# Optimization experiments

Measured on AMD Instinct MI355X. Metric: run time of the kernel, lower is better.

## Reference

```python
import jax, jax.numpy as jnp
import numpy as np
import math

D_MODEL = 512
N_HEADS = 8
WINDOW = 5
B, S = 4, 2048


def setup_inputs() -> dict:
    key = jax.random.key(0)
    ks = jax.random.split(key, 16)
    d = D_MODEL

    def lin(k, fan_in, fan_out):
        bound = 1.0 / math.sqrt(fan_in)
        kw, kb = jax.random.split(k)
        W = jax.random.uniform(kw, (fan_in, fan_out), jnp.float32, -bound, bound)
        b = jax.random.uniform(kb, (fan_out,), jnp.float32, -bound, bound)
        return W, b

    x = jax.random.normal(ks[0], (B, S, d), jnp.float32)
    W1, b1 = lin(ks[1], d, 2 * d)      # mapping layer 1
    W2, b2 = lin(ks[2], 2 * d, d)      # mapping layer 2
    Wq, bq = lin(ks[3], d, d)
    Wk, bk = lin(ks[4], d, d)
    Wv, bv = lin(ks[5], d, d)
    Wo, bo = lin(ks[6], d, d)
    return dict(x=x, W1=W1, b1=b1, W2=W2, b2=b2, Wq=Wq, bq=bq,
                Wk=Wk, bk=bk, Wv=Wv, bv=bv, Wo=Wo, bo=bo)


def reference(x, W1, b1, W2, b2, Wq, bq, Wk, bk, Wv, bv, Wo, bo):
    Bsz, S_, d = x.shape
    h = N_HEADS
    hd = d // h

    # mapping MLP: Linear -> ReLU -> Linear
    xm = jax.nn.relu(x @ W1 + b1) @ W2 + b2

    def split_heads(t):  # [B,S,d] -> [B,h,S,hd]
        return t.reshape(Bsz, S_, h, hd).transpose(0, 2, 1, 3)

    Q = split_heads(xm @ Wq + bq)
    K = split_heads(xm @ Wk + bk)
    V = split_heads(xm @ Wv + bv)

    scores = jnp.einsum('bhqd,bhkd->bhqk', Q, K) / math.sqrt(hd)

    # inverse sliding-window mask: positions with |i-j| <= window are EXCLUDED
    idx = jnp.arange(S_)
    adjacent = jnp.abs(idx[:, None] - idx[None, :]) <= WINDOW  # [S,S] bool
    scores = jnp.where(adjacent[None, None], -1e9, scores)

    attn = jax.nn.softmax(scores, axis=-1)
    out = jnp.einsum('bhqk,bhkd->bhqd', attn, V)
    out = out.transpose(0, 2, 1, 3).reshape(Bsz, S_, d)
    return out @ Wo + bo
```

## Files before the change

kernel.cpp:

```cpp
#include <hip/hip_runtime.h>
#include <stdint.h>

typedef __attribute__((ext_vector_type(8))) short bf16x8;
typedef __attribute__((ext_vector_type(4))) float f32x4;

__device__ __forceinline__ float bf2f(uint16_t u) {
    union { uint32_t u; float f; } c; c.u = ((uint32_t)u) << 16; return c.f;
}
__device__ __forceinline__ uint16_t f2bf(float f) {
    union { float f; uint32_t u; } c; c.f = f;
    uint32_t r = c.u + 0x7fffu + ((c.u >> 16) & 1u);
    return (uint16_t)(r >> 16);
}
__device__ __forceinline__ uint32_t pk2bf(float a, float b) {
#if __has_builtin(__builtin_amdgcn_cvt_pk_bf16_f32)
    auto v = __builtin_amdgcn_cvt_pk_bf16_f32(a, b);
    uint32_t u; __builtin_memcpy(&u, &v, 4); return u;
#else
    return (uint32_t)f2bf(a) | ((uint32_t)f2bf(b) << 16);
#endif
}
__device__ __forceinline__ float fexp2(float x) {
#if __has_builtin(__builtin_amdgcn_exp2f)
    return __builtin_amdgcn_exp2f(x);
#else
    return exp2f(x);
#endif
}

__device__ __forceinline__ void gld_lds16(const uint16_t* g, uint16_t* l) {
    __builtin_amdgcn_global_load_lds(
        (const __attribute__((address_space(1))) void*)g,
        (__attribute__((address_space(3))) void*)l, 16, 0, 0);
}

__global__ void prep_all(const float* __restrict__ x,
                         const float* __restrict__ W1, const float* __restrict__ W2,
                         const float* __restrict__ Wq, const float* __restrict__ Wk,
                         const float* __restrict__ Wv, const float* __restrict__ Wo,
                         const float* __restrict__ b1, const float* __restrict__ b2,
                         const float* __restrict__ bq, const float* __restrict__ bk,
                         const float* __restrict__ bv, const float* __restrict__ bo,
                         uint16_t* __restrict__ W1T, uint16_t* __restrict__ W2T,
                         uint16_t* __restrict__ WqkvT, uint16_t* __restrict__ WoT,
                         uint16_t* __restrict__ xb, uint16_t* __restrict__ bbase)
{
    const int id = blockIdx.x;
    const int tx = threadIdx.x, ty = threadIdx.y;
    const int tid = ty * 32 + tx;
    if (id < 2048) {
        __shared__ uint16_t t[32][33];
        const float* src; uint16_t* dst; int R, C, tile;
        if      (id < 512)  { src = W1; dst = W1T;              R = 512;  C = 1024; tile = id; }
        else if (id < 1024) { src = W2; dst = W2T;              R = 1024; C = 512;  tile = id - 512; }
        else if (id < 1280) { src = Wq; dst = WqkvT;            R = 512;  C = 512;  tile = id - 1024; }
        else if (id < 1536) { src = Wk; dst = WqkvT + 512*512;  R = 512;  C = 512;  tile = id - 1280; }
        else if (id < 1792) { src = Wv; dst = WqkvT + 1024*512; R = 512;  C = 512;  tile = id - 1536; }
        else                { src = Wo; dst = WoT;              R = 512;  C = 512;  tile = id - 1792; }
        const int ntx = C / 32;
        const int bx = (tile % ntx) * 32, by = (tile / ntx) * 32;
#pragma unroll
        for (int i = ty; i < 32; i += 8) t[i][tx] = f2bf(src[(size_t)(by + i) * C + bx + tx]);
        __syncthreads();
#pragma unroll
        for (int i = ty; i < 32; i += 8) dst[(size_t)(bx + i) * R + by + tx] = t[tx][i];
    } else if (id < 6144) {
        int i = (id - 2048) * 256 + tid;
        float4 v = ((const float4*)x)[i];
        ushort4 o;
        o.x = f2bf(v.x); o.y = f2bf(v.y); o.z = f2bf(v.z); o.w = f2bf(v.w);
        ((ushort4*)xb)[i] = o;
    } else {
        int i = (id - 6144) * 256 + tid;
        if      (i < 1024) bbase[i] = f2bf(b1[i]);
        else if (i < 1536) bbase[i] = f2bf(b2[i - 1024]);
        else if (i < 2048) bbase[i] = f2bf(bq[i - 1536]);
        else if (i < 2560) bbase[i] = f2bf(bk[i - 2048]);
        else if (i < 3072) bbase[i] = f2bf(bv[i - 2560]);
        else if (i < 3584) bbase[i] = f2bf(bo[i - 3072]);
    }
}

template<int RELU, int F32OUT>
__global__ __launch_bounds__(256, 3)
void gemm_k64(const uint16_t* __restrict__ A, const uint16_t* __restrict__ Bt,
              const uint16_t* __restrict__ bias, void* __restrict__ Cv,
              int M, int N, int K)
{
    __shared__ __align__(16) uint16_t lsA[2][64 * 64];
    __shared__ __align__(16) uint16_t lsB[2][128 * 64];

    const int tid = threadIdx.x, lane = tid & 63;
    const int wid = tid >> 6;
    const int quad = lane >> 4, lm = lane & 15;
    const int wm = wid >> 1, wn = wid & 1;
    const int m0 = blockIdx.y * 64, n0 = blockIdx.x * 128;

    f32x4 acc[2][4];
#pragma unroll
    for (int i = 0; i < 2; ++i)
#pragma unroll
        for (int j = 0; j < 4; ++j) acc[i][j] = (f32x4){0.f, 0.f, 0.f, 0.f};

    auto stage = [&](int k0, int bb) {
#pragma unroll
        for (int c4 = 0; c4 < 2; ++c4) {
            const int chunk = c4 * 256 + tid;
            const int r = chunk >> 3, lc = (chunk & 7) ^ (r & 7);
            gld_lds16(A + (size_t)(m0 + r) * K + k0 + lc * 8, &lsA[bb][(size_t)chunk * 8]);
        }
#pragma unroll
        for (int c4 = 0; c4 < 4; ++c4) {
            const int chunk = c4 * 256 + tid;
            const int r = chunk >> 3, lc = (chunk & 7) ^ (r & 7);
            gld_lds16(Bt + (size_t)(n0 + r) * K + k0 + lc * 8, &lsB[bb][(size_t)chunk * 8]);
        }
    };
    auto compute = [&](int bb) {
#pragma unroll
        for (int kh = 0; kh < 2; ++kh) {
            const int pc = ((kh * 4 + quad) ^ (lm & 7));
            bf16x8 af[2], bfr[4];
#pragma unroll
            for (int t = 0; t < 2; ++t)
                af[t] = *(const bf16x8*)(&lsA[bb][(wm * 32 + t * 16 + lm) * 64 + pc * 8]);
#pragma unroll
            for (int t = 0; t < 4; ++t)
                bfr[t] = *(const bf16x8*)(&lsB[bb][(wn * 64 + t * 16 + lm) * 64 + pc * 8]);
#pragma unroll
            for (int i = 0; i < 2; ++i)
#pragma unroll
                for (int j = 0; j < 4; ++j)
                    acc[i][j] = __builtin_amdgcn_mfma_f32_16x16x32_bf16(af[i], bfr[j], acc[i][j], 0, 0, 0);
        }
    };

    stage(0, 0);
    int cur = 0;
#pragma unroll 1
    for (int k0 = 64; k0 < K; k0 += 64) {
        stage(k0, cur ^ 1);
        asm volatile("s_waitcnt vmcnt(6)" ::: "memory");
        __builtin_amdgcn_sched_barrier(0);
        __builtin_amdgcn_s_barrier();
        compute(cur);
        __builtin_amdgcn_s_barrier();
        cur ^= 1;
    }
    asm volatile("s_waitcnt vmcnt(0)" ::: "memory");
    __builtin_amdgcn_sched_barrier(0);
    __builtin_amdgcn_s_barrier();
    compute(cur);

#pragma unroll
    for (int i = 0; i < 2; ++i) {
        const int r0 = m0 + wm * 32 + i * 16 + quad * 4;
#pragma unroll
        for (int j = 0; j < 4; ++j) {
            const int col = n0 + wn * 64 + j * 16 + lm;
            const float bvj = bf2f(bias[col]);
#pragma unroll
            for (int r = 0; r < 4; ++r) {
                float v = acc[i][j][r] + bvj;
                if (RELU) v = fmaxf(v, 0.f);
                if (F32OUT) ((float*)Cv)[(size_t)(r0 + r) * N + col] = v;
                else        ((uint16_t*)Cv)[(size_t)(r0 + r) * N + col] = f2bf(v);
            }
        }
    }
}

template<int RELU, int F32OUT>
__global__ __launch_bounds__(256, 4)
void gemm_k32(const uint16_t* __restrict__ A, const uint16_t* __restrict__ Bt,
              const uint16_t* __restrict__ bias, void* __restrict__ Cv,
              int M, int N, int K)
{
    __shared__ __align__(16) uint16_t lsA[2][32 * 64];
    __shared__ __align__(16) uint16_t lsB[2][128 * 64];

    const int tid = threadIdx.x, lane = tid & 63;
    const int wid = tid >> 6;
    const int quad = lane >> 4, lm = lane & 15;
    const int wm = wid >> 1, wn = wid & 1;
    const int m0 = blockIdx.y * 32, n0 = blockIdx.x * 128;

    f32x4 acc[4];
#pragma unroll
    for (int j = 0; j < 4; ++j) acc[j] = (f32x4){0.f, 0.f, 0.f, 0.f};

    auto stage = [&](int k0, int bb) {
        {
            const int chunk = tid;
            const int r = chunk >> 3, lc = (chunk & 7) ^ (r & 7);
            gld_lds16(A + (size_t)(m0 + r) * K + k0 + lc * 8, &lsA[bb][(size_t)chunk * 8]);
        }
#pragma unroll
        for (int c4 = 0; c4 < 4; ++c4) {
            const int chunk = c4 * 256 + tid;
            const int r = chunk >> 3, lc = (chunk & 7) ^ (r & 7);
            gld_lds16(Bt + (size_t)(n0 + r) * K + k0 + lc * 8, &lsB[bb][(size_t)chunk * 8]);
        }
    };
    auto compute = [&](int bb) {
#pragma unroll
        for (int kh = 0; kh < 2; ++kh) {
            const int pc = ((kh * 4 + quad) ^ (lm & 7));
            bf16x8 af = *(const bf16x8*)(&lsA[bb][(wm * 16 + lm) * 64 + pc * 8]);
            bf16x8 bfr[4];
#pragma unroll
            for (int t = 0; t < 4; ++t)
                bfr[t] = *(const bf16x8*)(&lsB[bb][(wn * 64 + t * 16 + lm) * 64 + pc * 8]);
#pragma unroll
            for (int j = 0; j < 4; ++j)
                acc[j] = __builtin_amdgcn_mfma_f32_16x16x32_bf16(af, bfr[j], acc[j], 0, 0, 0);
        }
    };

    stage(0, 0);
    int cur = 0;
#pragma unroll 1
    for (int k0 = 64; k0 < K; k0 += 64) {
        stage(k0, cur ^ 1);
        asm volatile("s_waitcnt vmcnt(5)" ::: "memory");
        __builtin_amdgcn_sched_barrier(0);
        __builtin_amdgcn_s_barrier();
        compute(cur);
        __builtin_amdgcn_s_barrier();
        cur ^= 1;
    }
    asm volatile("s_waitcnt vmcnt(0)" ::: "memory");
    __builtin_amdgcn_sched_barrier(0);
    __builtin_amdgcn_s_barrier();
    compute(cur);

    const int r0 = m0 + wm * 16 + quad * 4;
#pragma unroll
    for (int j = 0; j < 4; ++j) {
        const int col = n0 + wn * 64 + j * 16 + lm;
        const float bvj = bf2f(bias[col]);
#pragma unroll
        for (int r = 0; r < 4; ++r) {
            float v = acc[j][r] + bvj;
            if (RELU) v = fmaxf(v, 0.f);
            if (F32OUT) ((float*)Cv)[(size_t)(r0 + r) * N + col] = v;
            else        ((uint16_t*)Cv)[(size_t)(r0 + r) * N + col] = f2bf(v);
        }
    }
}

__global__ __launch_bounds__(256, 3)
void gemm_qkv64(const uint16_t* __restrict__ A, const uint16_t* __restrict__ Bt,
                const uint16_t* __restrict__ bq, const uint16_t* __restrict__ bk,
                const uint16_t* __restrict__ bv_,
                uint16_t* __restrict__ qk, uint16_t* __restrict__ Vt)
{
    __shared__ __align__(16) uint16_t lsA[2][64 * 64];
    __shared__ __align__(16) uint16_t lsB[2][128 * 64];

    const int tid = threadIdx.x, lane = tid & 63;
    const int wid = tid >> 6;
    const int quad = lane >> 4, lm = lane & 15;
    const int wm = wid >> 1, wn = wid & 1;
    const int m0 = blockIdx.y * 64, n0 = blockIdx.x * 128;
    const int part = n0 >> 9;
    const uint16_t* B = (part == 0) ? bq : (part == 1) ? bk : bv_;
    const int K = 512;

    f32x4 acc[2][4];
#pragma unroll
    for (int i = 0; i < 2; ++i)
#pragma unroll
        for (int j = 0; j < 4; ++j) acc[i][j] = (f32x4){0.f, 0.f, 0.f, 0.f};

    auto stage = [&](int k0, int bb) {
#pragma unroll
        for (int c4 = 0; c4 < 2; ++c4) {
            const int chunk = c4 * 256 + tid;
            const int r = chunk >> 3, lc = (chunk & 7) ^ (r & 7);
            gld_lds16(A + (size_t)(m0 + r) * K + k0 + lc * 8, &lsA[bb][(size_t)chunk * 8]);
        }
#pragma unroll
        for (int c4 = 0; c4 < 4; ++c4) {
            const int chunk = c4 * 256 + tid;
            const int r = chunk >> 3, lc = (chunk & 7) ^ (r & 7);
            gld_lds16(Bt + (size_t)(n0 + r) * K + k0 + lc * 8, &lsB[bb][(size_t)chunk * 8]);
        }
    };
    auto compute = [&](int bb) {
#pragma unroll
        for (int kh = 0; kh < 2; ++kh) {
            const int pc = ((kh * 4 + quad) ^ (lm & 7));
            bf16x8 af[2], bfr[4];
#pragma unroll
            for (int t = 0; t < 2; ++t)
                af[t] = *(const bf16x8*)(&lsA[bb][(wm * 32 + t * 16 + lm) * 64 + pc * 8]);
#pragma unroll
            for (int t = 0; t < 4; ++t)
                bfr[t] = *(const bf16x8*)(&lsB[bb][(wn * 64 + t * 16 + lm) * 64 + pc * 8]);
#pragma unroll
            for (int i = 0; i < 2; ++i)
#pragma unroll
                for (int j = 0; j < 4; ++j)
                    acc[i][j] = __builtin_amdgcn_mfma_f32_16x16x32_bf16(af[i], bfr[j], acc[i][j], 0, 0, 0);
        }
    };

    stage(0, 0);
    int cur = 0;
#pragma unroll 1
    for (int k0 = 64; k0 < K; k0 += 64) {
        stage(k0, cur ^ 1);
        asm volatile("s_waitcnt vmcnt(6)" ::: "memory");
        __builtin_amdgcn_sched_barrier(0);
        __builtin_amdgcn_s_barrier();
        compute(cur);
        __builtin_amdgcn_s_barrier();
        cur ^= 1;
    }
    asm volatile("s_waitcnt vmcnt(0)" ::: "memory");
    __builtin_amdgcn_sched_barrier(0);
    __builtin_amdgcn_s_barrier();
    compute(cur);

#pragma unroll
    for (int i = 0; i < 2; ++i) {
        const int mb = m0 + wm * 32 + i * 16 + quad * 4;
#pragma unroll
        for (int j = 0; j < 4; ++j) {
            const int nl = (n0 & 511) + wn * 64 + j * 16 + lm;
            const float bvj = bf2f(B[nl]);
            if (part < 2) {
#pragma unroll
                for (int r = 0; r < 4; ++r)
                    qk[(size_t)(mb + r) * 1024 + part * 512 + nl] = f2bf(acc[i][j][r] + bvj);
            } else {
                const int h = nl >> 6, d = nl & 63;
                const int b = mb >> 11, s0 = mb & 2047;
                const int sp = (s0 & ~31) | ((s0 & 12) << 1) | (((s0 >> 4) & 1) << 2);
                const size_t base = ((size_t)(((b << 3) | h)) * 64 + d) * 2048 + sp;
#pragma unroll
                for (int r = 0; r < 4; ++r)
                    Vt[base + r] = f2bf(acc[i][j][r] + bvj);
            }
        }
    }
}

__global__ __launch_bounds__(512, 4)
void attn_k(const uint16_t* __restrict__ qk, const uint16_t* __restrict__ Vt,
            uint16_t* __restrict__ Out)
{
    __shared__ __align__(16) uint16_t lsAll[2][16384];

    const int tid = threadIdx.x, lane = tid & 63, wid = tid >> 6;
    const int qw = wid & 3, kh2 = wid >> 2;
    const int quad = lane >> 4, lm = lane & 15;
    const int bh = blockIdx.y, b = bh >> 3, h = bh & 7;
    const int q0 = blockIdx.x * 128;
    const float cscale = 0.125f * 1.44269504088896f;

    bf16x8 qf[2][2];
#pragma unroll
    for (int i = 0; i < 2; ++i)
#pragma unroll
        for (int ks = 0; ks < 2; ++ks) {
            bf16x8 q = *(const bf16x8*)(qk +
                (size_t)(b * 2048 + q0 + qw * 32 + i * 16 + lm) * 1024 + h * 64 + ks * 32 + quad * 8);
#pragma unroll
            for (int e = 0; e < 8; ++e)
                q[e] = (short)f2bf(bf2f((uint16_t)q[e]) * cscale);
            qf[i][ks] = q;
        }

    f32x4 oacc[2][4];
#pragma unroll
    for (int i = 0; i < 2; ++i)
#pragma unroll
        for (int n = 0; n < 4; ++n) oacc[i][n] = (f32x4){0.f, 0.f, 0.f, 0.f};
    float lrow[2] = {0.f, 0.f};

    auto stage = [&](int j0, int bb) {
        uint16_t* lsK = &lsAll[bb][0];
        uint16_t* lsV = &lsAll[bb][8192];
#pragma unroll
        for (int c2 = 0; c2 < 2; ++c2) {
            const int chunk = c2 * 512 + tid;
            const int r = chunk >> 3, lc = (chunk & 7) ^ (r & 7);
            gld_lds16(qk + (size_t)(b * 2048 + j0 + r) * 1024 + 512 + h * 64 + lc * 8,
                      lsK + (size_t)chunk * 8);
        }
#pragma unroll
        for (int c2 = 0; c2 < 2; ++c2) {
            const int chunk = c2 * 512 + tid;
            const int d = chunk >> 4, lc = (chunk & 15) ^ (d & 15);
            gld_lds16(Vt + (size_t)(bh * 64 + d) * 2048 + j0 + lc * 8,
                      lsV + (size_t)chunk * 8);
        }
    };

    auto compute = [&](int j0, int bb) {
        const uint16_t* Kb = &lsAll[bb][0];
        const uint16_t* Vb = &lsAll[bb][8192];

        f32x4 sacc[2][4];
#pragma unroll
        for (int i = 0; i < 2; ++i)
#pragma unroll
            for (int j = 0; j < 4; ++j) sacc[i][j] = (f32x4){0.f, 0.f, 0.f, 0.f};
        __builtin_amdgcn_s_setprio(1);
#pragma unroll
        for (int ks = 0; ks < 2; ++ks)
#pragma unroll
            for (int j = 0; j < 4; ++j) {
                const int pc = (ks * 4 + quad) ^ (lm & 7);
                bf16x8 kf = *(const bf16x8*)(Kb + (kh2 * 64 + j * 16 + lm) * 64 + pc * 8);
#pragma unroll
                for (int i = 0; i < 2; ++i)
                    sacc[i][j] = __builtin_amdgcn_mfma_f32_16x16x32_bf16(kf, qf[i][ks], sacc[i][j], 0, 0, 0);
            }
        __builtin_amdgcn_s_setprio(0);

        if ((j0 + 127 >= q0 - 5) && (j0 <= q0 + 127 + 5)) {
#pragma unroll
            for (int i = 0; i < 2; ++i) {
                const int qr = q0 + qw * 32 + i * 16 + lm;
#pragma unroll
                for (int j = 0; j < 4; ++j)
#pragma unroll
                    for (int r = 0; r < 4; ++r) {
                        int kc = j0 + kh2 * 64 + j * 16 + quad * 4 + r;
                        int dd = qr - kc; if (dd < 0) dd = -dd;
                        if (dd <= 5) sacc[i][j][r] = -1e30f;
                    }
            }
        }

#pragma unroll
        for (int ksl = 0; ksl < 2; ++ksl) {
            const int gs = kh2 * 2 + ksl;
            bf16x8 pa[2];
#pragma unroll
            for (int i = 0; i < 2; ++i) {
                const float p0 = fexp2(sacc[i][2 * ksl + 0][0]);
                const float p1 = fexp2(sacc[i][2 * ksl + 0][1]);
                const float p2 = fexp2(sacc[i][2 * ksl + 0][2]);
                const float p3 = fexp2(sacc[i][2 * ksl + 0][3]);
                const float p4 = fexp2(sacc[i][2 * ksl + 1][0]);
                const float p5 = fexp2(sacc[i][2 * ksl + 1][1]);
                const float p6 = fexp2(sacc[i][2 * ksl + 1][2]);
                const float p7 = fexp2(sacc[i][2 * ksl + 1][3]);
                lrow[i] += ((p0 + p1) + (p2 + p3)) + ((p4 + p5) + (p6 + p7));
                union { bf16x8 v; uint32_t u[4]; } c;
                c.u[0] = pk2bf(p0, p1);
                c.u[1] = pk2bf(p2, p3);
                c.u[2] = pk2bf(p4, p5);
                c.u[3] = pk2bf(p6, p7);
                pa[i] = c.v;
            }
            __builtin_amdgcn_s_setprio(1);
#pragma unroll
            for (int n = 0; n < 4; ++n) {
                const int pc = (gs * 4 + quad) ^ lm;
                bf16x8 vf = *(const bf16x8*)(Vb + (n * 16 + lm) * 128 + pc * 8);
#pragma unroll
                for (int i = 0; i < 2; ++i)
                    oacc[i][n] = __builtin_amdgcn_mfma_f32_16x16x32_bf16(pa[i], vf, oacc[i][n], 0, 0, 0);
            }
            __builtin_amdgcn_s_setprio(0);
        }
    };

    stage(0, 0);
    int cur = 0;
#pragma unroll 1
    for (int jt = 0; jt < 15; ++jt) {
        stage((jt + 1) * 128, cur ^ 1);
        asm volatile("s_waitcnt vmcnt(4)" ::: "memory");
        __builtin_amdgcn_sched_barrier(0);
        __builtin_amdgcn_s_barrier();
        compute(jt * 128, cur);
        __builtin_amdgcn_s_barrier();
        cur ^= 1;
    }
    asm volatile("s_waitcnt vmcnt(0)" ::: "memory");
    __builtin_amdgcn_sched_barrier(0);
    __builtin_amdgcn_s_barrier();
    compute(15 * 128, cur);

    __syncthreads();
    f32x4* red = (f32x4*)&lsAll[0][0];
    if (wid >= 4) {
        const int base = ((wid - 4) * 64 + lane) * 9;
#pragma unroll
        for (int i = 0; i < 2; ++i)
#pragma unroll
            for (int n = 0; n < 4; ++n) red[base + i * 4 + n] = oacc[i][n];
        red[base + 8] = (f32x4){lrow[0], lrow[1], 0.f, 0.f};
    }
    __syncthreads();
    if (wid < 4) {
        const int base = (wid * 64 + lane) * 9;
#pragma unroll
        for (int i = 0; i < 2; ++i)
#pragma unroll
            for (int n = 0; n < 4; ++n) oacc[i][n] += red[base + i * 4 + n];
        const f32x4 lr = red[base + 8];
        lrow[0] += lr[0]; lrow[1] += lr[1];

#pragma unroll
        for (int i = 0; i < 2; ++i) {
            float l = lrow[i];
            l += __shfl_xor(l, 16);
            l += __shfl_xor(l, 32);
            const float inv = 1.f / (l + 1e-30f);
#pragma unroll
            for (int r = 0; r < 4; ++r) {
                const float invr = __shfl(inv, quad * 4 + r, 16);
                const int s = q0 + wid * 32 + i * 16 + quad * 4 + r;
#pragma unroll
                for (int n = 0; n < 4; ++n)
                    Out[(size_t)(b * 2048 + s) * 512 + h * 64 + n * 16 + lm] = f2bf(oacc[i][n][r] * invr);
            }
        }
    }
}

extern "C" void kernel_launch(void* const* d_in, const int* in_sizes, int n_in,
                              void* d_out, int out_size, void* d_ws, size_t ws_size,
                              hipStream_t stream)
{
    const float* x  = (const float*)d_in[0];
    const float* W1 = (const float*)d_in[1];
    const float* b1 = (const float*)d_in[2];
    const float* W2 = (const float*)d_in[3];
    const float* b2 = (const float*)d_in[4];
    const float* Wq = (const float*)d_in[5];
    const float* bq = (const float*)d_in[6];
    const float* Wk = (const float*)d_in[7];
    const float* bk = (const float*)d_in[8];
    const float* Wv = (const float*)d_in[9];
    const float* bv = (const float*)d_in[10];
    const float* Wo = (const float*)d_in[11];
    const float* bo = (const float*)d_in[12];
    (void)in_sizes; (void)n_in; (void)out_size; (void)ws_size;

    char* ws = (char*)d_ws;
    const size_t MiB = 1024 * 1024;
    uint16_t* xb    = (uint16_t*)(ws + 0);
    uint16_t* W1T   = (uint16_t*)(ws + 8 * MiB);
    uint16_t* W2T   = (uint16_t*)(ws + 9 * MiB);
    uint16_t* WqkvT = (uint16_t*)(ws + 10 * MiB);
    uint16_t* WoT   = (uint16_t*)(ws + 11 * MiB + 512 * 1024);
    uint16_t* bbase = (uint16_t*)(ws + 12 * MiB);
    uint16_t* b1b = bbase, *b2b = bbase + 1024, *bqb = bbase + 1536;
    uint16_t* bkb = bbase + 2048, *bvb = bbase + 2560, *bob = bbase + 3072;
    uint16_t* xm1   = (uint16_t*)(ws + 13 * MiB);
    uint16_t* xm    = (uint16_t*)(ws + 29 * MiB);
    uint16_t* qk    = xm1;
    uint16_t* att   = xm;
    uint16_t* Vt    = xb;

    prep_all<<<6158, dim3(32, 8), 0, stream>>>(x, W1, W2, Wq, Wk, Wv, Wo,
                                               b1, b2, bq, bk, bv, bo,
                                               W1T, W2T, WqkvT, WoT, xb, bbase);

    gemm_k64<1,0><<<dim3(8, 128),  256, 0, stream>>>(xb,  W1T, b1b, xm1, 8192, 1024, 512);
    gemm_k32<0,0><<<dim3(4, 256),  256, 0, stream>>>(xm1, W2T, b2b, xm,  8192, 512, 1024);
    gemm_qkv64   <<<dim3(12, 128), 256, 0, stream>>>(xm, WqkvT, bqb, bkb, bvb, qk, Vt);
    attn_k       <<<dim3(16, 32),  512, 0, stream>>>(qk, Vt, att);
    gemm_k32<0,1><<<dim3(4, 256),  256, 0, stream>>>(att, WoT, bob, d_out, 8192, 512, 512);
}
```

Baseline: 211.6 us.

## Fold W2 into QKV weights, stage V transpose through LDS, remap attention blocks

Since the second mapping layer is linear, W2 is folded into Wq/Wk/Wv. A small GEMM builds the combined 1536x1024 weight, and the combined biases b2·W + b are computed in prep. This removes the 8192x512x1024 GEMM and the xm round trip, and the QKV GEMM now runs with K=1024 directly on the ReLU output. The V output is transposed through LDS so it can be written as 16-byte vector stores instead of scattered 2-byte stores. Attention blocks are remapped so each XCD handles contiguous batch-heads for better L2 locality. The trade-offs are changed rounding, since the combined weights are quantised to bf16, and a serial fp32 bias dot product in prep.

```diff
diff --git a/kernel.cpp b/kernel.cpp
--- a/kernel.cpp
+++ b/kernel.cpp
@@ -41,18 +41,26 @@
                          const float* __restrict__ b1, const float* __restrict__ b2,
                          const float* __restrict__ bq, const float* __restrict__ bk,
                          const float* __restrict__ bv, const float* __restrict__ bo,
-                         uint16_t* __restrict__ W1T, uint16_t* __restrict__ W2T,
+                         uint16_t* __restrict__ W1T, uint16_t* __restrict__ W2b,
                          uint16_t* __restrict__ WqkvT, uint16_t* __restrict__ WoT,
-                         uint16_t* __restrict__ xb, uint16_t* __restrict__ bbase)
+                         uint16_t* __restrict__ xb, uint16_t* __restrict__ bbase,
+                         float* __restrict__ bcf)
 {
     const int id = blockIdx.x;
     const int tx = threadIdx.x, ty = threadIdx.y;
     const int tid = ty * 32 + tx;
     if (id < 2048) {
+        if (id >= 512 && id < 1024) {
+            const int t2 = id - 512;
+            const int bx = (t2 & 15) * 32, by = (t2 >> 4) * 32;
+#pragma unroll
+            for (int i = ty; i < 32; i += 8)
+                W2b[(size_t)(by + i) * 512 + bx + tx] = f2bf(W2[(size_t)(by + i) * 512 + bx + tx]);
+            return;
+        }
         __shared__ uint16_t t[32][33];
         const float* src; uint16_t* dst; int R, C, tile;
         if      (id < 512)  { src = W1; dst = W1T;              R = 512;  C = 1024; tile = id; }
-        else if (id < 1024) { src = W2; dst = W2T;              R = 1024; C = 512;  tile = id - 512; }
         else if (id < 1280) { src = Wq; dst = WqkvT;            R = 512;  C = 512;  tile = id - 1024; }
         else if (id < 1536) { src = Wk; dst = WqkvT + 512*512;  R = 512;  C = 512;  tile = id - 1280; }
         else if (id < 1792) { src = Wv; dst = WqkvT + 1024*512; R = 512;  C = 512;  tile = id - 1536; }
@@ -70,7 +78,7 @@
         ushort4 o;
         o.x = f2bf(v.x); o.y = f2bf(v.y); o.z = f2bf(v.z); o.w = f2bf(v.w);
         ((ushort4*)xb)[i] = o;
-    } else {
+    } else if (id < 6162) {
         int i = (id - 6144) * 256 + tid;
         if      (i < 1024) bbase[i] = f2bf(b1[i]);
         else if (i < 1536) bbase[i] = f2bf(b2[i - 1024]);
@@ -78,6 +86,15 @@
         else if (i < 2560) bbase[i] = f2bf(bk[i - 2048]);
         else if (i < 3072) bbase[i] = f2bf(bv[i - 2560]);
         else if (i < 3584) bbase[i] = f2bf(bo[i - 3072]);
+        else if (i < 4608) bbase[i] = 0;
+    } else {
+        const int n = (id - 6162) * 256 + tid;
+        const int part = n >> 9, col = n & 511;
+        const float* W = (part == 0) ? Wq : (part == 1) ? Wk : Wv;
+        float s = ((part == 0) ? bq : (part == 1) ? bk : bv)[col];
+#pragma unroll 4
+        for (int j = 0; j < 512; ++j) s += b2[j] * W[(size_t)j * 512 + col];
+        bcf[n] = s;
     }
 }
 
@@ -251,8 +268,7 @@
 
 __global__ __launch_bounds__(256, 3)
 void gemm_qkv64(const uint16_t* __restrict__ A, const uint16_t* __restrict__ Bt,
-                const uint16_t* __restrict__ bq, const uint16_t* __restrict__ bk,
-                const uint16_t* __restrict__ bv_,
+                const float* __restrict__ bc,
                 uint16_t* __restrict__ qk, uint16_t* __restrict__ Vt)
 {
     __shared__ __align__(16) uint16_t lsA[2][64 * 64];
@@ -264,8 +280,7 @@
     const int wm = wid >> 1, wn = wid & 1;
     const int m0 = blockIdx.y * 64, n0 = blockIdx.x * 128;
     const int part = n0 >> 9;
-    const uint16_t* B = (part == 0) ? bq : (part == 1) ? bk : bv_;
-    const int K = 512;
+    const int K = 1024;
 
     f32x4 acc[2][4];
 #pragma unroll
@@ -323,26 +338,45 @@
     __builtin_amdgcn_s_barrier();
     compute(cur);
 
-#pragma unroll
-    for (int i = 0; i < 2; ++i) {
-        const int mb = m0 + wm * 32 + i * 16 + quad * 4;
-#pragma unroll
-        for (int j = 0; j < 4; ++j) {
-            const int nl = (n0 & 511) + wn * 64 + j * 16 + lm;
-            const float bvj = bf2f(B[nl]);
-            if (part < 2) {
+    if (part < 2) {
+#pragma unroll
+        for (int i = 0; i < 2; ++i) {
+            const int mb = m0 + wm * 32 + i * 16 + quad * 4;
+#pragma unroll
+            for (int j = 0; j < 4; ++j) {
+                const int nl = (n0 & 511) + wn * 64 + j * 16 + lm;
+                const float bvj = bc[part * 512 + nl];
 #pragma unroll
                 for (int r = 0; r < 4; ++r)
                     qk[(size_t)(mb + r) * 1024 + part * 512 + nl] = f2bf(acc[i][j][r] + bvj);
-            } else {
-                const int h = nl >> 6, d = nl & 63;
-                const int b = mb >> 11, s0 = mb & 2047;
-                const int sp = (s0 & ~31) | ((s0 & 12) << 1) | (((s0 >> 4) & 1) << 2);
-                const size_t base = ((size_t)(((b << 3) | h)) * 64 + d) * 2048 + sp;
-#pragma unroll
-                for (int r = 0; r < 4; ++r)
-                    Vt[base + r] = f2bf(acc[i][j][r] + bvj);
-            }
+            }
+        }
+    } else {
+        __syncthreads();
+        uint16_t* tb = &lsB[0][0];
+#pragma unroll
+        for (int i = 0; i < 2; ++i) {
+#pragma unroll
+            for (int j = 0; j < 4; ++j) {
+                const int hd = wn * 64 + j * 16 + lm;
+                const float bvj = bc[1024 + (n0 & 511) + hd];
+#pragma unroll
+                for (int r = 0; r < 4; ++r) {
+                    const int kk = wm * 32 + i * 16 + quad * 4 + r;
+                    const int kp = (kk & 32) | ((kk & 12) << 1) | (((kk >> 4) & 1) << 2) | (kk & 3);
+                    tb[hd * 64 + (kp ^ ((hd & 7) << 3))] = f2bf(acc[i][j][r] + bvj);
+                }
+            }
+        }
+        __syncthreads();
+        const int b = m0 >> 11, s0 = m0 & 2047, h0 = (n0 & 511) >> 6;
+#pragma unroll
+        for (int t2 = 0; t2 < 4; ++t2) {
+            const int task = t2 * 256 + tid;
+            const int hd = task >> 3, seg = task & 7;
+            const bf16x8 v = *(const bf16x8*)(tb + hd * 64 + ((seg ^ (hd & 7)) << 3));
+            const int hh = h0 + (hd >> 6), d = hd & 63;
+            *(bf16x8*)(Vt + ((size_t)((b << 3) | hh) * 64 + d) * 2048 + s0 + seg * 8) = v;
         }
     }
 }
@@ -356,8 +390,10 @@
     const int tid = threadIdx.x, lane = tid & 63, wid = tid >> 6;
     const int qw = wid & 3, kh2 = wid >> 2;
     const int quad = lane >> 4, lm = lane & 15;
-    const int bh = blockIdx.y, b = bh >> 3, h = bh & 7;
-    const int q0 = blockIdx.x * 128;
+    const int ib = blockIdx.y * 16 + blockIdx.x;
+    const int xcd = ib & 7, kq = ib >> 3;
+    const int bh = xcd * 4 + (kq >> 4), q0 = (kq & 15) * 128;
+    const int b = bh >> 3, h = bh & 7;
     const float cscale = 0.125f * 1.44269504088896f;
 
     bf16x8 qf[2][2];
@@ -549,25 +585,25 @@
     const size_t MiB = 1024 * 1024;
     uint16_t* xb    = (uint16_t*)(ws + 0);
     uint16_t* W1T   = (uint16_t*)(ws + 8 * MiB);
-    uint16_t* W2T   = (uint16_t*)(ws + 9 * MiB);
+    uint16_t* W2b   = (uint16_t*)(ws + 9 * MiB);
     uint16_t* WqkvT = (uint16_t*)(ws + 10 * MiB);
     uint16_t* WoT   = (uint16_t*)(ws + 11 * MiB + 512 * 1024);
     uint16_t* bbase = (uint16_t*)(ws + 12 * MiB);
-    uint16_t* b1b = bbase, *b2b = bbase + 1024, *bqb = bbase + 1536;
-    uint16_t* bkb = bbase + 2048, *bvb = bbase + 2560, *bob = bbase + 3072;
+    uint16_t* b1b = bbase, *bob = bbase + 3072, *bzero = bbase + 3584;
+    float*    bcf   = (float*)(ws + 12 * MiB + 32 * 1024);
     uint16_t* xm1   = (uint16_t*)(ws + 13 * MiB);
-    uint16_t* xm    = (uint16_t*)(ws + 29 * MiB);
-    uint16_t* qk    = xm1;
-    uint16_t* att   = xm;
+    uint16_t* WcT   = (uint16_t*)(ws + 29 * MiB);
+    uint16_t* att   = (uint16_t*)(ws + 29 * MiB);
     uint16_t* Vt    = xb;
-
-    prep_all<<<6158, dim3(32, 8), 0, stream>>>(x, W1, W2, Wq, Wk, Wv, Wo,
+    uint16_t* qk    = (uint16_t*)d_out;
+
+    prep_all<<<6168, dim3(32, 8), 0, stream>>>(x, W1, W2, Wq, Wk, Wv, Wo,
                                                b1, b2, bq, bk, bv, bo,
-                                               W1T, W2T, WqkvT, WoT, xb, bbase);
-
-    gemm_k64<1,0><<<dim3(8, 128),  256, 0, stream>>>(xb,  W1T, b1b, xm1, 8192, 1024, 512);
-    gemm_k32<0,0><<<dim3(4, 256),  256, 0, stream>>>(xm1, W2T, b2b, xm,  8192, 512, 1024);
-    gemm_qkv64   <<<dim3(12, 128), 256, 0, stream>>>(xm, WqkvT, bqb, bkb, bvb, qk, Vt);
+                                               W1T, W2b, WqkvT, WoT, xb, bbase, bcf);
+
+    gemm_k64<1,0><<<dim3(8, 128), 256, 0, stream>>>(xb, W1T, b1b, xm1, 8192, 1024, 512);
+    gemm_k64<0,0><<<dim3(8, 24),  256, 0, stream>>>(WqkvT, W2b, bzero, WcT, 1536, 1024, 512);
+    gemm_qkv64   <<<dim3(12, 128), 256, 0, stream>>>(xm1, WcT, bcf, qk, Vt);
     attn_k       <<<dim3(16, 32),  512, 0, stream>>>(qk, Vt, att);
     gemm_k32<0,1><<<dim3(4, 256),  256, 0, stream>>>(att, WoT, bob, d_out, 8192, 512, 512);
 }
```

After: 249.6 us. +18.0%, slower.

## Fuse x bf16 conversion into first GEMM, stage V transpose in LDS, remap attention blocks

Applied to the files above, without the earlier changes.

The separate x fp32-to-bf16 conversion pass is removed. The first GEMM now loads fp32 x through registers, converts it, and writes it to LDS, overlapping that work with compute. The V-output epilogue of the QKV GEMM now transposes through LDS so it writes coalesced 16-byte vectors instead of scattered 2-byte stores. Attention blocks are remapped so each XCD handles a contiguous set of heads, which should improve L2 locality. The cost is more register pressure and extra barriers in the first GEMM.

```diff
diff --git a/kernel.cpp b/kernel.cpp
--- a/kernel.cpp
+++ b/kernel.cpp
@@ -34,8 +34,7 @@
         (__attribute__((address_space(3))) void*)l, 16, 0, 0);
 }
 
-__global__ void prep_all(const float* __restrict__ x,
-                         const float* __restrict__ W1, const float* __restrict__ W2,
+__global__ void prep_all(const float* __restrict__ W1, const float* __restrict__ W2,
                          const float* __restrict__ Wq, const float* __restrict__ Wk,
                          const float* __restrict__ Wv, const float* __restrict__ Wo,
                          const float* __restrict__ b1, const float* __restrict__ b2,
@@ -43,7 +42,7 @@
                          const float* __restrict__ bv, const float* __restrict__ bo,
                          uint16_t* __restrict__ W1T, uint16_t* __restrict__ W2T,
                          uint16_t* __restrict__ WqkvT, uint16_t* __restrict__ WoT,
-                         uint16_t* __restrict__ xb, uint16_t* __restrict__ bbase)
+                         uint16_t* __restrict__ bbase)
 {
     const int id = blockIdx.x;
     const int tx = threadIdx.x, ty = threadIdx.y;
@@ -64,14 +63,8 @@
         __syncthreads();
 #pragma unroll
         for (int i = ty; i < 32; i += 8) dst[(size_t)(bx + i) * R + by + tx] = t[tx][i];
-    } else if (id < 6144) {
+    } else {
         int i = (id - 2048) * 256 + tid;
-        float4 v = ((const float4*)x)[i];
-        ushort4 o;
-        o.x = f2bf(v.x); o.y = f2bf(v.y); o.z = f2bf(v.z); o.w = f2bf(v.w);
-        ((ushort4*)xb)[i] = o;
-    } else {
-        int i = (id - 6144) * 256 + tid;
         if      (i < 1024) bbase[i] = f2bf(b1[i]);
         else if (i < 1536) bbase[i] = f2bf(b2[i - 1024]);
         else if (i < 2048) bbase[i] = f2bf(bq[i - 1536]);
@@ -81,11 +74,9 @@
     }
 }
 
-template<int RELU, int F32OUT>
 __global__ __launch_bounds__(256, 3)
-void gemm_k64(const uint16_t* __restrict__ A, const uint16_t* __restrict__ Bt,
-              const uint16_t* __restrict__ bias, void* __restrict__ Cv,
-              int M, int N, int K)
+void gemm_g1(const float* __restrict__ Af, const uint16_t* __restrict__ Bt,
+             const uint16_t* __restrict__ bias, uint16_t* __restrict__ C)
 {
     __shared__ __align__(16) uint16_t lsA[2][64 * 64];
     __shared__ __align__(16) uint16_t lsB[2][128 * 64];
@@ -95,6 +86,7 @@
     const int quad = lane >> 4, lm = lane & 15;
     const int wm = wid >> 1, wn = wid & 1;
     const int m0 = blockIdx.y * 64, n0 = blockIdx.x * 128;
+    const int K = 512, N = 1024;
 
     f32x4 acc[2][4];
 #pragma unroll
@@ -102,13 +94,30 @@
 #pragma unroll
         for (int j = 0; j < 4; ++j) acc[i][j] = (f32x4){0.f, 0.f, 0.f, 0.f};
 
-    auto stage = [&](int k0, int bb) {
-#pragma unroll
-        for (int c4 = 0; c4 < 2; ++c4) {
-            const int chunk = c4 * 256 + tid;
+    float4 ald[2][2];
+    auto stage_load = [&](int k0) {
+#pragma unroll
+        for (int c2 = 0; c2 < 2; ++c2) {
+            const int chunk = c2 * 256 + tid;
             const int r = chunk >> 3, lc = (chunk & 7) ^ (r & 7);
-            gld_lds16(A + (size_t)(m0 + r) * K + k0 + lc * 8, &lsA[bb][(size_t)chunk * 8]);
-        }
+            const float4* src = (const float4*)(Af + (size_t)(m0 + r) * K + k0 + lc * 8);
+            ald[c2][0] = src[0];
+            ald[c2][1] = src[1];
+        }
+    };
+    auto stage_write = [&](int bb) {
+#pragma unroll
+        for (int c2 = 0; c2 < 2; ++c2) {
+            const int chunk = c2 * 256 + tid;
+            union { bf16x8 v; uint32_t u[4]; } c;
+            c.u[0] = pk2bf(ald[c2][0].x, ald[c2][0].y);
+            c.u[1] = pk2bf(ald[c2][0].z, ald[c2][0].w);
+            c.u[2] = pk2bf(ald[c2][1].x, ald[c2][1].y);
+            c.u[3] = pk2bf(ald[c2][1].z, ald[c2][1].w);
+            *(bf16x8*)(&lsA[bb][(size_t)chunk * 8]) = c.v;
+        }
+    };
+    auto stage_B = [&](int k0, int bb) {
 #pragma unroll
         for (int c4 = 0; c4 < 4; ++c4) {
             const int chunk = c4 * 256 + tid;
@@ -135,19 +144,28 @@
         }
     };
 
-    stage(0, 0);
+    stage_load(0);
+    stage_B(0, 0);
+    stage_write(0);
+    asm volatile("s_waitcnt vmcnt(0) lgkmcnt(0)" ::: "memory");
+    __builtin_amdgcn_sched_barrier(0);
+    __builtin_amdgcn_s_barrier();
+
     int cur = 0;
 #pragma unroll 1
     for (int k0 = 64; k0 < K; k0 += 64) {
-        stage(k0, cur ^ 1);
-        asm volatile("s_waitcnt vmcnt(6)" ::: "memory");
+        stage_load(k0);
+        stage_B(k0, cur ^ 1);
+        asm volatile("s_waitcnt vmcnt(12)" ::: "memory");
         __builtin_amdgcn_sched_barrier(0);
         __builtin_amdgcn_s_barrier();
         compute(cur);
+        stage_write(cur ^ 1);
+        asm volatile("s_waitcnt lgkmcnt(0)" ::: "memory");
         __builtin_amdgcn_s_barrier();
         cur ^= 1;
     }
-    asm volatile("s_waitcnt vmcnt(0)" ::: "memory");
+    asm volatile("s_waitcnt vmcnt(0) lgkmcnt(0)" ::: "memory");
     __builtin_amdgcn_sched_barrier(0);
     __builtin_amdgcn_s_barrier();
     compute(cur);
@@ -161,10 +179,8 @@
             const float bvj = bf2f(bias[col]);
 #pragma unroll
             for (int r = 0; r < 4; ++r) {
-                float v = acc[i][j][r] + bvj;
-                if (RELU) v = fmaxf(v, 0.f);
-                if (F32OUT) ((float*)Cv)[(size_t)(r0 + r) * N + col] = v;
-                else        ((uint16_t*)Cv)[(size_t)(r0 + r) * N + col] = f2bf(v);
+                float v = fmaxf(acc[i][j][r] + bvj, 0.f);
+                C[(size_t)(r0 + r) * N + col] = f2bf(v);
             }
         }
     }
@@ -323,26 +339,45 @@
     __builtin_amdgcn_s_barrier();
     compute(cur);
 
-#pragma unroll
-    for (int i = 0; i < 2; ++i) {
-        const int mb = m0 + wm * 32 + i * 16 + quad * 4;
-#pragma unroll
-        for (int j = 0; j < 4; ++j) {
-            const int nl = (n0 & 511) + wn * 64 + j * 16 + lm;
-            const float bvj = bf2f(B[nl]);
-            if (part < 2) {
+    if (part < 2) {
+#pragma unroll
+        for (int i = 0; i < 2; ++i) {
+            const int mb = m0 + wm * 32 + i * 16 + quad * 4;
+#pragma unroll
+            for (int j = 0; j < 4; ++j) {
+                const int nl = (n0 & 511) + wn * 64 + j * 16 + lm;
+                const float bvj = bf2f(B[nl]);
 #pragma unroll
                 for (int r = 0; r < 4; ++r)
                     qk[(size_t)(mb + r) * 1024 + part * 512 + nl] = f2bf(acc[i][j][r] + bvj);
-            } else {
-                const int h = nl >> 6, d = nl & 63;
-                const int b = mb >> 11, s0 = mb & 2047;
-                const int sp = (s0 & ~31) | ((s0 & 12) << 1) | (((s0 >> 4) & 1) << 2);
-                const size_t base = ((size_t)(((b << 3) | h)) * 64 + d) * 2048 + sp;
-#pragma unroll
-                for (int r = 0; r < 4; ++r)
-                    Vt[base + r] = f2bf(acc[i][j][r] + bvj);
-            }
+            }
+        }
+    } else {
+        __syncthreads();
+        uint16_t* tb = &lsB[0][0];
+#pragma unroll
+        for (int i = 0; i < 2; ++i) {
+#pragma unroll
+            for (int j = 0; j < 4; ++j) {
+                const int hd = wn * 64 + j * 16 + lm;
+                const float bvj = bf2f(B[(n0 & 511) + hd]);
+#pragma unroll
+                for (int r = 0; r < 4; ++r) {
+                    const int kk = wm * 32 + i * 16 + quad * 4 + r;
+                    const int kp = (kk & 32) | ((kk & 12) << 1) | (((kk >> 4) & 1) << 2) | (kk & 3);
+                    tb[hd * 64 + (kp ^ ((hd & 7) << 3))] = f2bf(acc[i][j][r] + bvj);
+                }
+            }
+        }
+        __syncthreads();
+        const int b = m0 >> 11, s0 = m0 & 2047, h0 = (n0 & 511) >> 6;
+#pragma unroll
+        for (int t2 = 0; t2 < 4; ++t2) {
+            const int task = t2 * 256 + tid;
+            const int hd = task >> 3, seg = task & 7;
+            const bf16x8 v = *(const bf16x8*)(tb + hd * 64 + ((seg ^ (hd & 7)) << 3));
+            const int hh = h0 + (hd >> 6), d = hd & 63;
+            *(bf16x8*)(Vt + ((size_t)((b << 3) | hh) * 64 + d) * 2048 + s0 + seg * 8) = v;
         }
     }
 }
@@ -356,8 +391,10 @@
     const int tid = threadIdx.x, lane = tid & 63, wid = tid >> 6;
     const int qw = wid & 3, kh2 = wid >> 2;
     const int quad = lane >> 4, lm = lane & 15;
-    const int bh = blockIdx.y, b = bh >> 3, h = bh & 7;
-    const int q0 = blockIdx.x * 128;
+    const int ib = blockIdx.y * 16 + blockIdx.x;
+    const int xcd = ib & 7, kq = ib >> 3;
+    const int bh = xcd * 4 + (kq >> 4), q0 = (kq & 15) * 128;
+    const int b = bh >> 3, h = bh & 7;
     const float cscale = 0.125f * 1.44269504088896f;
 
     bf16x8 qf[2][2];
@@ -547,7 +584,7 @@
 
     char* ws = (char*)d_ws;
     const size_t MiB = 1024 * 1024;
-    uint16_t* xb    = (uint16_t*)(ws + 0);
+    uint16_t* Vt    = (uint16_t*)(ws + 0);
     uint16_t* W1T   = (uint16_t*)(ws + 8 * MiB);
     uint16_t* W2T   = (uint16_t*)(ws + 9 * MiB);
     uint16_t* WqkvT = (uint16_t*)(ws + 10 * MiB);
@@ -559,14 +596,13 @@
     uint16_t* xm    = (uint16_t*)(ws + 29 * MiB);
     uint16_t* qk    = xm1;
     uint16_t* att   = xm;
-    uint16_t* Vt    = xb;
-
-    prep_all<<<6158, dim3(32, 8), 0, stream>>>(x, W1, W2, Wq, Wk, Wv, Wo,
+
+    prep_all<<<2062, dim3(32, 8), 0, stream>>>(W1, W2, Wq, Wk, Wv, Wo,
                                                b1, b2, bq, bk, bv, bo,
-                                               W1T, W2T, WqkvT, WoT, xb, bbase);
-
-    gemm_k64<1,0><<<dim3(8, 128),  256, 0, stream>>>(xb,  W1T, b1b, xm1, 8192, 1024, 512);
-    gemm_k32<0,0><<<dim3(4, 256),  256, 0, stream>>>(xm1, W2T, b2b, xm,  8192, 512, 1024);
+                                               W1T, W2T, WqkvT, WoT, bbase);
+
+    gemm_g1      <<<dim3(8, 128),  256, 0, stream>>>(x, W1T, b1b, xm1);
+    gemm_k32<0,0><<<dim3(4, 256),  256, 0, stream>>>(xm1, W2T, b2b, xm, 8192, 512, 1024);
     gemm_qkv64   <<<dim3(12, 128), 256, 0, stream>>>(xm, WqkvT, bqb, bkb, bvb, qk, Vt);
     attn_k       <<<dim3(16, 32),  512, 0, stream>>>(qk, Vt, att);
     gemm_k32<0,1><<<dim3(4, 256),  256, 0, stream>>>(att, WoT, bob, d_out, 8192, 512, 512);
```

Result: slower. 223.8 us (+5.8%).

## Swizzle block indices per XCD and stage V transpose through LDS

Applied to the files above, without the earlier changes.

Remaps linear block ids so blocks that share A rows or the same (batch, head) run on the same XCD. The aim is better L2 reuse on the multi-die GPU, for the GEMMs and for attention. The QKV GEMM epilogue now writes the V tile transposed into shared memory, then stores it with coalesced 16-byte writes instead of scattered 2-byte stores. The swizzle assumes gridDim.y is divisible by 8 and the attention grid is 16x32, and the LDS staging adds two barriers.

```diff
diff --git a/kernel.cpp b/kernel.cpp
--- a/kernel.cpp
+++ b/kernel.cpp
@@ -32,6 +32,14 @@
     __builtin_amdgcn_global_load_lds(
         (const __attribute__((address_space(1))) void*)g,
         (__attribute__((address_space(3))) void*)l, 16, 0, 0);
+}
+
+__device__ __forceinline__ int2 xcd_swz() {
+    const int nx = gridDim.x;
+    const int ib = blockIdx.y * nx + blockIdx.x;
+    const int c = ib & 7, j = ib >> 3;
+    const int mpx = gridDim.y >> 3;
+    return make_int2(c * mpx + j / nx, j % nx);
 }
 
 __global__ void prep_all(const float* __restrict__ x,
@@ -94,7 +102,8 @@
     const int wid = tid >> 6;
     const int quad = lane >> 4, lm = lane & 15;
     const int wm = wid >> 1, wn = wid & 1;
-    const int m0 = blockIdx.y * 64, n0 = blockIdx.x * 128;
+    const int2 sw = xcd_swz();
+    const int m0 = sw.x * 64, n0 = sw.y * 128;
 
     f32x4 acc[2][4];
 #pragma unroll
@@ -183,7 +192,8 @@
     const int wid = tid >> 6;
     const int quad = lane >> 4, lm = lane & 15;
     const int wm = wid >> 1, wn = wid & 1;
-    const int m0 = blockIdx.y * 32, n0 = blockIdx.x * 128;
+    const int2 sw = xcd_swz();
+    const int m0 = sw.x * 32, n0 = sw.y * 128;
 
     f32x4 acc[4];
 #pragma unroll
@@ -262,7 +272,8 @@
     const int wid = tid >> 6;
     const int quad = lane >> 4, lm = lane & 15;
     const int wm = wid >> 1, wn = wid & 1;
-    const int m0 = blockIdx.y * 64, n0 = blockIdx.x * 128;
+    const int2 sw = xcd_swz();
+    const int m0 = sw.x * 64, n0 = sw.y * 128;
     const int part = n0 >> 9;
     const uint16_t* B = (part == 0) ? bq : (part == 1) ? bk : bv_;
     const int K = 512;
@@ -323,26 +334,45 @@
     __builtin_amdgcn_s_barrier();
     compute(cur);
 
-#pragma unroll
-    for (int i = 0; i < 2; ++i) {
-        const int mb = m0 + wm * 32 + i * 16 + quad * 4;
-#pragma unroll
-        for (int j = 0; j < 4; ++j) {
-            const int nl = (n0 & 511) + wn * 64 + j * 16 + lm;
-            const float bvj = bf2f(B[nl]);
-            if (part < 2) {
+    if (part < 2) {
+#pragma unroll
+        for (int i = 0; i < 2; ++i) {
+            const int mb = m0 + wm * 32 + i * 16 + quad * 4;
+#pragma unroll
+            for (int j = 0; j < 4; ++j) {
+                const int nl = (n0 & 511) + wn * 64 + j * 16 + lm;
+                const float bvj = bf2f(B[nl]);
 #pragma unroll
                 for (int r = 0; r < 4; ++r)
                     qk[(size_t)(mb + r) * 1024 + part * 512 + nl] = f2bf(acc[i][j][r] + bvj);
-            } else {
-                const int h = nl >> 6, d = nl & 63;
-                const int b = mb >> 11, s0 = mb & 2047;
-                const int sp = (s0 & ~31) | ((s0 & 12) << 1) | (((s0 >> 4) & 1) << 2);
-                const size_t base = ((size_t)(((b << 3) | h)) * 64 + d) * 2048 + sp;
-#pragma unroll
-                for (int r = 0; r < 4; ++r)
-                    Vt[base + r] = f2bf(acc[i][j][r] + bvj);
-            }
+            }
+        }
+    } else {
+        __syncthreads();
+        uint16_t* tb = &lsB[0][0];
+#pragma unroll
+        for (int i = 0; i < 2; ++i) {
+#pragma unroll
+            for (int j = 0; j < 4; ++j) {
+                const int hd = wn * 64 + j * 16 + lm;
+                const float bvj = bf2f(B[(n0 & 511) + hd]);
+#pragma unroll
+                for (int r = 0; r < 4; ++r) {
+                    const int kk = wm * 32 + i * 16 + quad * 4 + r;
+                    const int kp = (kk & 32) | ((kk & 12) << 1) | (((kk >> 4) & 1) << 2) | (kk & 3);
+                    tb[hd * 64 + (kp ^ ((hd & 7) << 3))] = f2bf(acc[i][j][r] + bvj);
+                }
+            }
+        }
+        __syncthreads();
+        const int b = m0 >> 11, s0 = m0 & 2047, h0 = (n0 & 511) >> 6;
+#pragma unroll
+        for (int t2 = 0; t2 < 4; ++t2) {
+            const int task = t2 * 256 + tid;
+            const int hd = task >> 3, seg = task & 7;
+            const bf16x8 v = *(const bf16x8*)(tb + hd * 64 + ((seg ^ (hd & 7)) << 3));
+            const int hh = h0 + (hd >> 6), d = hd & 63;
+            *(bf16x8*)(Vt + ((size_t)((b << 3) | hh) * 64 + d) * 2048 + s0 + seg * 8) = v;
         }
     }
 }
@@ -356,8 +386,10 @@
     const int tid = threadIdx.x, lane = tid & 63, wid = tid >> 6;
     const int qw = wid & 3, kh2 = wid >> 2;
     const int quad = lane >> 4, lm = lane & 15;
-    const int bh = blockIdx.y, b = bh >> 3, h = bh & 7;
-    const int q0 = blockIdx.x * 128;
+    const int ib = blockIdx.y * 16 + blockIdx.x;
+    const int xcd = ib & 7, kq = ib >> 3;
+    const int bh = xcd * 4 + (kq >> 4), q0 = (kq & 15) * 128;
+    const int b = bh >> 3, h = bh & 7;
     const float cscale = 0.125f * 1.44269504088896f;
 
     bf16x8 qf[2][2];
```

New measurement: 206.2 us (median of 3 runs). 2.6% less time.
